# Optimization experiments

Hardware: AMD Instinct MI355X
Metric: run time of the kernel (lower is better)

## Reference

```python
import jax, jax.numpy as jnp
import numpy as np

N_NODES = 50000
N_EDGES = 1600000
IN_DIM, HID_DIM, OUT_DIM, HEADS = 128, 128, 64, 8
NEG_SLOPE = 0.2
BN_EPS = 1e-5


def setup_inputs() -> dict:
    key = jax.random.key(0)
    ks = jax.random.split(key, 12)
    hpc = HID_DIM // HEADS  # per-head channels of layer 1
    return {
        "x": jax.random.normal(ks[0], (N_NODES, IN_DIM), jnp.float32),
        "edge_index": jax.random.randint(ks[1], (2, N_EDGES), 0, N_NODES, jnp.int64),
        "W1": jax.random.normal(ks[2], (IN_DIM, HEADS * hpc), jnp.float32) * 0.05,
        "a1_src": jax.random.normal(ks[3], (HEADS, hpc), jnp.float32) * 0.1,
        "a1_dst": jax.random.normal(ks[4], (HEADS, hpc), jnp.float32) * 0.1,
        "b1": jnp.zeros((HEADS * hpc,), jnp.float32),
        "bn_gamma": jnp.ones((HID_DIM,), jnp.float32),
        "bn_beta": jnp.zeros((HID_DIM,), jnp.float32),
        "W2": jax.random.normal(ks[5], (HID_DIM, OUT_DIM), jnp.float32) * 0.05,
        "a2_src": jax.random.normal(ks[6], (1, OUT_DIM), jnp.float32) * 0.1,
        "a2_dst": jax.random.normal(ks[7], (1, OUT_DIM), jnp.float32) * 0.1,
        "b2": jnp.zeros((OUT_DIM,), jnp.float32),
    }


def _gat_conv(x, src, dst, W, a_src, a_dst, bias, heads, n_nodes):
    # x: [N, Fin]; src/dst: [E'] (self-loops already appended)
    hpc = W.shape[1] // heads
    h = (x @ W).reshape(n_nodes, heads, hpc)                 # [N,H,C]
    alpha_s = jnp.einsum("nhc,hc->nh", h, a_src)             # [N,H]
    alpha_d = jnp.einsum("nhc,hc->nh", h, a_dst)
    e = alpha_s[src] + alpha_d[dst]                          # [E',H]
    e = jax.nn.leaky_relu(e, NEG_SLOPE)
    # segment softmax over destination neighborhoods
    m = jax.ops.segment_max(e, dst, num_segments=n_nodes)    # [N,H]
    m = jnp.where(jnp.isfinite(m), m, 0.0)
    ee = jnp.exp(e - m[dst])
    denom = jax.ops.segment_sum(ee, dst, num_segments=n_nodes)
    alpha = ee / (denom[dst] + 1e-16)                        # [E',H]
    msg = h[src] * alpha[:, :, None]                         # [E',H,C]
    out = jax.ops.segment_sum(msg, dst, num_segments=n_nodes)  # [N,H,C]
    return out.reshape(n_nodes, heads * hpc) + bias


def _batch_norm(x, gamma, beta):
    mu = jnp.mean(x, axis=0)
    var = jnp.var(x, axis=0)
    return gamma * (x - mu) * jax.lax.rsqrt(var + BN_EPS) + beta


def reference(x, edge_index, W1, a1_src, a1_dst, b1, bn_gamma, bn_beta, W2, a2_src, a2_dst, b2):
    n = x.shape[0]
    loops = jnp.arange(n, dtype=edge_index.dtype)
    src = jnp.concatenate([edge_index[0], loops])            # PyG add_self_loops
    dst = jnp.concatenate([edge_index[1], loops])
    h = _gat_conv(x, src, dst, W1, a1_src, a1_dst, b1, HEADS, n)
    h = _batch_norm(h, bn_gamma, bn_beta)
    h = jax.nn.elu(h)
    # dropout: identity at inference
    out = _gat_conv(h, src, dst, W2, a2_src, a2_dst, b2, 1, n)
    return out
```

## Files before the change

kernel.cpp:

```cpp
#include <hip/hip_runtime.h>
#include <hip/hip_bf16.h>

#define N_NODES 50000
#define N_EDGES 1600000
#define HEADS 8
#define NBK 196
#define NBLK 196
#define EPB 8192

typedef unsigned short u16;
typedef unsigned char u8;
typedef unsigned int u32;
typedef __attribute__((ext_vector_type(8))) short bf16x8;
typedef __attribute__((ext_vector_type(4))) float f32x4;

__device__ __forceinline__ float bf2f(u16 u) {
  union { u32 i; float f; } v; v.i = ((u32)u) << 16; return v.f;
}
__device__ __forceinline__ float bflo(u32 p) {
  union { u32 i; float f; } v; v.i = p << 16; return v.f;
}
__device__ __forceinline__ float bfhi(u32 p) {
  union { u32 i; float f; } v; v.i = p & 0xffff0000u; return v.f;
}
__device__ __forceinline__ u16 f2bf(float f) {
  union { float f; u32 i; } v; v.f = f;
  u32 r = v.i + 0x7fff + ((v.i >> 16) & 1);
  return (u16)(r >> 16);
}
__device__ __forceinline__ u32 pack2(float a, float b) {
  return (u32)f2bf(a) | ((u32)f2bf(b) << 16);
}

__global__ void k_detect(const u16* __restrict__ x, const u32* __restrict__ ei,
                         int* __restrict__ flags) {
  __shared__ int cbig, cnz;
  if (threadIdx.x == 0) { cbig = 0; cnz = 0; }
  __syncthreads();
  int lb = 0, ln = 0;
  for (int i = threadIdx.x; i < 4096; i += 256) {
    int ex = (x[i] >> 7) & 0xff;
    lb += (ex >= 140);
    if (i < 2048) ln += (ei[2 * i + 1] != 0);
  }
  atomicAdd(&cbig, lb); atomicAdd(&cnz, ln);
  __syncthreads();
  if (threadIdx.x == 0) {
    flags[0] = (cbig > 16) ? 1 : 0;
    flags[1] = (cnz == 0) ? 1 : 0;
  }
}

__global__ void k_convsmall(const void* a1s, const void* a1d, const void* b1,
                            const void* gam, const void* bet, const void* a2s,
                            const void* a2d, const void* b2, const void* W1,
                            const void* W2, float* __restrict__ smallf,
                            u16* __restrict__ w1t, u16* __restrict__ w2t,
                            const int* __restrict__ flags) {
  int i = blockIdx.x * 256 + threadIdx.x;
  if (i >= 25408) return;
  bool f32 = flags[0] != 0;
  auto ld = [&](const void* p, int off) -> float {
    return f32 ? ((const float*)p)[off] : bf2f(((const u16*)p)[off]);
  };
  if (i >= 17216) {
    int j = i - 17216, n = j >> 7, k = j & 127;
    w2t[j] = f2bf(ld(W2, k * 64 + n));
  } else if (i >= 832) {
    int j = i - 832, n = j >> 7, k = j & 127;
    w1t[j] = f2bf(ld(W1, k * 128 + n));
  } else {
    const void* src; int off;
    if (i >= 768)      { src = b2;  off = i - 768; }
    else if (i >= 704) { src = a2d; off = i - 704; }
    else if (i >= 640) { src = a2s; off = i - 640; }
    else if (i >= 512) { src = bet; off = i - 512; }
    else if (i >= 384) { src = gam; off = i - 384; }
    else if (i >= 256) { src = b1;  off = i - 256; }
    else if (i >= 128) { src = a1d; off = i - 128; }
    else               { src = a1s; off = i; }
    smallf[i] = ld(src, off);
  }
}

__global__ __launch_bounds__(256) void k_hist(const int* __restrict__ ei,
                                              int* __restrict__ H,
                                              int* __restrict__ totals,
                                              const int* __restrict__ flags) {
  __shared__ int hist[NBK];
  int t = threadIdx.x, blk = blockIdx.x;
  for (int i = t; i < NBK; i += 256) hist[i] = 0;
  __syncthreads();
  bool i64 = flags[1] != 0;
  int base = blk * EPB;
  for (int k = 0; k < 32; k++) {
    int e = base + k * 256 + t;
    if (e < N_EDGES) {
      int d = i64 ? ei[2 * (N_EDGES + e)] : ei[N_EDGES + e];
      atomicAdd(&hist[d >> 8], 1);
    }
  }
  __syncthreads();
  for (int i = t; i < NBK; i += 256) {
    H[i * NBLK + blk] = hist[i];
    atomicAdd(&totals[i], hist[i]);
  }
}

__global__ void k_scan_tot(const int* __restrict__ totals, int* __restrict__ bucketBase) {
  __shared__ int tmp[256];
  int t = threadIdx.x;
  int v = (t < NBK) ? totals[t] : 0;
  tmp[t] = v; __syncthreads();
  for (int o = 1; o < 256; o <<= 1) {
    int x = (t >= o) ? tmp[t - o] : 0; __syncthreads();
    tmp[t] += x; __syncthreads();
  }
  if (t < NBK) bucketBase[t] = tmp[t] - v;
  if (t == NBK - 1) bucketBase[NBK] = tmp[t];
}

__global__ void k_scan_blk(const int* __restrict__ H, const int* __restrict__ bucketBase,
                           int* __restrict__ P) {
  __shared__ int tmp[256];
  int t = threadIdx.x, b = blockIdx.x;
  int v = (t < NBLK) ? H[b * NBLK + t] : 0;
  tmp[t] = v; __syncthreads();
  for (int o = 1; o < 256; o <<= 1) {
    int x = (t >= o) ? tmp[t - o] : 0; __syncthreads();
    tmp[t] += x; __syncthreads();
  }
  if (t < NBLK) P[b * NBLK + t] = bucketBase[b] + tmp[t] - v;
}

__global__ __launch_bounds__(256) void k_bucket(const int* __restrict__ ei,
                                                const int* __restrict__ P,
                                                u32* __restrict__ buf,
                                                const int* __restrict__ flags) {
  __shared__ u32 sv[EPB];
  __shared__ u16 rank[EPB];
  __shared__ u8  sk8[EPB];
  __shared__ int cnt[NBK], scn[NBK], tmp[256];
  int t = threadIdx.x, blk = blockIdx.x;
  int base = blk * EPB;
  int nE = N_EDGES - base; if (nE > EPB) nE = EPB;
  for (int i = t; i < NBK; i += 256) cnt[i] = 0;
  __syncthreads();
  bool i64 = flags[1] != 0;
  for (int k = 0; k < EPB / 256; k++) {
    int li = k * 256 + t, e = base + li;
    if (li < nE) {
      int d = i64 ? ei[2 * (N_EDGES + e)] : ei[N_EDGES + e];
      rank[li] = (u16)atomicAdd(&cnt[d >> 8], 1);
    }
  }
  __syncthreads();
  int v = (t < NBK) ? cnt[t] : 0;
  tmp[t] = v; __syncthreads();
  for (int o = 1; o < 256; o <<= 1) {
    int x = (t >= o) ? tmp[t - o] : 0; __syncthreads();
    tmp[t] += x; __syncthreads();
  }
  if (t < NBK) scn[t] = tmp[t] - v;
  __syncthreads();
  for (int k = 0; k < EPB / 256; k++) {
    int li = k * 256 + t, e = base + li;
    if (li < nE) {
      int s = i64 ? ei[2 * e] : ei[e];
      int d = i64 ? ei[2 * (N_EDGES + e)] : ei[N_EDGES + e];
      int key = d >> 8;
      int pos = scn[key] + rank[li];
      sv[pos] = ((u32)(d & 255) << 16) | (u32)s;
      sk8[pos] = (u8)key;
    }
  }
  __syncthreads();
  for (int i = t; i < nE; i += 256) {
    int b = sk8[i];
    buf[P[b * NBLK + blk] + (i - scn[b])] = sv[i];
  }
}

__global__ __launch_bounds__(256) void k_csr(const u32* __restrict__ buf,
                                             const int* __restrict__ bucketBase,
                                             int* __restrict__ row_start,
                                             int* __restrict__ deg,
                                             int* __restrict__ csr, int N) {
  __shared__ int cnt[256], scn[256], cur[256];
  int b = blockIdx.x, t = threadIdx.x;
  int lo = bucketBase[b], hi = bucketBase[b + 1];
  cnt[t] = 0; __syncthreads();
  for (int e = lo + t; e < hi; e += 256) atomicAdd(&cnt[(buf[e] >> 16) & 255], 1);
  __syncthreads();
  int v = cnt[t];
  scn[t] = v; __syncthreads();
  for (int o = 1; o < 256; o <<= 1) {
    int x = (t >= o) ? scn[t - o] : 0; __syncthreads();
    scn[t] += x; __syncthreads();
  }
  int excl = scn[t] - v;
  int node = b * 256 + t;
  if (node < N) { row_start[node] = lo + excl; deg[node] = v; }
  cur[t] = lo + excl;
  __syncthreads();
  for (int e = lo + t; e < hi; e += 256) {
    u32 p = buf[e];
    int pos = atomicAdd(&cur[(p >> 16) & 255], 1);
    csr[pos] = p & 0xffff;
  }
}

template <int NCOLS, bool EPI, bool AFLAG>
__global__ __launch_bounds__(256) void k_gemm_mfma(const void* __restrict__ A,
                                                   const u16* __restrict__ BT,
                                                   const float* __restrict__ scale,
                                                   const float* __restrict__ shift,
                                                   const float* __restrict__ a2s,
                                                   const float* __restrict__ a2d,
                                                   float* __restrict__ as_out,
                                                   float* __restrict__ ad_out,
                                                   u16* __restrict__ C, int M,
                                                   const int* __restrict__ flags) {
  constexpr int KP = 136;
  constexpr int NT = NCOLS / 16;
  __shared__ u16 As[64 * KP];
  __shared__ u16 Bs[NCOLS * KP];
  int t = threadIdx.x;
  int row0 = blockIdx.x * 64;
  bool af32 = AFLAG ? (flags[0] != 0) : false;

  for (int i = t; i < NCOLS * 16; i += 256) {
    int n = i >> 4, q = i & 15;
    *(uint4*)&Bs[n * KP + q * 8] = ((const uint4*)BT)[n * 16 + q];
  }
  for (int i = t; i < 64 * 32; i += 256) {
    int r = i >> 5, c4 = i & 31;
    int row = row0 + r;
    uint2 pk = make_uint2(0u, 0u);
    if (row < M) {
      if (EPI) {
        uint2 p = ((const uint2*)A)[(size_t)row * 32 + c4];
        int c = c4 * 4;
        float v0 = bflo(p.x), v1 = bfhi(p.x), v2 = bflo(p.y), v3 = bfhi(p.y);
        v0 = fmaf(v0, scale[c],     shift[c]);     v0 = v0 > 0.f ? v0 : __expf(v0) - 1.f;
        v1 = fmaf(v1, scale[c + 1], shift[c + 1]); v1 = v1 > 0.f ? v1 : __expf(v1) - 1.f;
        v2 = fmaf(v2, scale[c + 2], shift[c + 2]); v2 = v2 > 0.f ? v2 : __expf(v2) - 1.f;
        v3 = fmaf(v3, scale[c + 3], shift[c + 3]); v3 = v3 > 0.f ? v3 : __expf(v3) - 1.f;
        pk.x = pack2(v0, v1); pk.y = pack2(v2, v3);
      } else if (af32) {
        float4 v = ((const float4*)A)[(size_t)row * 32 + c4];
        pk.x = pack2(v.x, v.y); pk.y = pack2(v.z, v.w);
      } else {
        pk = ((const uint2*)A)[(size_t)row * 32 + c4];
      }
    }
    *(uint2*)&As[r * KP + c4 * 4] = pk;
  }
  __syncthreads();

  int lane = t & 63, w = t >> 6;
  int m = lane & 15, quad = lane >> 4;
  f32x4 acc[NT];
#pragma unroll
  for (int nt = 0; nt < NT; nt++) acc[nt] = (f32x4)(0.f);
  const u16* aBase = &As[(w * 16 + m) * KP + quad * 8];
  const u16* bBase = &Bs[m * KP + quad * 8];
#pragma unroll
  for (int ks = 0; ks < 4; ks++) {
    bf16x8 af = *(const bf16x8*)(aBase + ks * 32);
#pragma unroll
    for (int nt = 0; nt < NT; nt++) {
      bf16x8 bf = *(const bf16x8*)(bBase + nt * 16 * KP + ks * 32);
      acc[nt] = __builtin_amdgcn_mfma_f32_16x16x32_bf16(af, bf, acc[nt], 0, 0, 0);
    }
  }
  int orow0 = row0 + w * 16 + quad * 4;
#pragma unroll
  for (int nt = 0; nt < NT; nt++) {
#pragma unroll
    for (int r = 0; r < 4; r++) {
      int row = orow0 + r;
      if (row < M) C[(size_t)row * NCOLS + nt * 16 + m] = f2bf(acc[nt][r]);
    }
  }
  if (EPI) {
    float a2sv[NT], a2dv[NT];
#pragma unroll
    for (int nt = 0; nt < NT; nt++) { a2sv[nt] = a2s[nt * 16 + m]; a2dv[nt] = a2d[nt * 16 + m]; }
#pragma unroll
    for (int r = 0; r < 4; r++) {
      float vs = 0.f, vd = 0.f;
#pragma unroll
      for (int nt = 0; nt < NT; nt++) {
        vs = fmaf(acc[nt][r], a2sv[nt], vs);
        vd = fmaf(acc[nt][r], a2dv[nt], vd);
      }
      vs += __shfl_xor(vs, 1); vd += __shfl_xor(vd, 1);
      vs += __shfl_xor(vs, 2); vd += __shfl_xor(vd, 2);
      vs += __shfl_xor(vs, 4); vd += __shfl_xor(vd, 4);
      vs += __shfl_xor(vs, 8); vd += __shfl_xor(vd, 8);
      int row = orow0 + r;
      if (row < M && m == 0) { as_out[row] = vs; ad_out[row] = vd; }
    }
  }
}

__global__ void k_alpha1(const u16* __restrict__ h1b, const float* __restrict__ a1s,
                         const float* __restrict__ a1d, float* __restrict__ as_out,
                         float* __restrict__ ad_out, int N) {
  int idx = blockIdx.x * 256 + threadIdx.x;
  if (idx >= N * HEADS) return;
  int n = idx >> 3, h = idx & 7;
  const u32* hp = (const u32*)&h1b[((size_t)n << 7) + (h << 4)];
  float s = 0.f, d = 0.f;
#pragma unroll
  for (int q = 0; q < 8; q++) {
    u32 p = hp[q];
    float v0 = bflo(p), v1 = bfhi(p);
    int b = (h << 4) + q * 2;
    s = fmaf(v0, a1s[b], s); s = fmaf(v1, a1s[b + 1], s);
    d = fmaf(v0, a1d[b], d); d = fmaf(v1, a1d[b + 1], d);
  }
  as_out[idx] = s; ad_out[idx] = d;
}

__global__ __launch_bounds__(256) void k_agg1(const u16* __restrict__ h1b,
                                              const float* __restrict__ as_,
                                              const float* __restrict__ ad_,
                                              const int* __restrict__ csr,
                                              const int* __restrict__ row_start,
                                              const int* __restrict__ deg,
                                              const float* __restrict__ b1,
                                              u16* __restrict__ out, int N) {
  int node = blockIdx.x * 4 + (threadIdx.x >> 6);
  if (node >= N) return;
  int l = threadIdx.x & 63;
  int head = l >> 3, sub = l & 7;
  int gbase = l & 56;
  int node_u = __builtin_amdgcn_readfirstlane(node);
  int st = __builtin_amdgcn_readfirstlane(row_start[node_u]);
  int cnt = __builtin_amdgcn_readfirstlane(deg[node_u]);
  const int* cp = csr + st;
  const u32* h32 = (const u32*)h1b;
  float ad = ad_[(node_u << 3) | head];
  float sp = 0.f, a0 = 0.f, a1 = 0.f;
  int j = 0;
  for (; j + 8 <= cnt; j += 8) {
    int ssub = cp[j + sub];
    float e = as_[(ssub << 3) | head] + ad;
    e = fmaxf(e, 0.2f * e);
    float p = __expf(e);
    sp += p;
#pragma unroll
    for (int k = 0; k < 8; k++) {
      int sk = cp[j + k];
      float pk = __shfl(p, gbase | k);
      u32 hv = h32[(sk << 6) | l];
      a0 = fmaf(pk, bflo(hv), a0);
      a1 = fmaf(pk, bfhi(hv), a1);
    }
  }
  for (; j < cnt; j++) {
    int s0 = cp[j];
    float e0 = as_[(s0 << 3) | head] + ad;
    e0 = fmaxf(e0, 0.2f * e0);
    float p0 = __expf(e0);
    if (sub == 0) sp += p0;
    u32 hv = h32[(s0 << 6) | l];
    a0 = fmaf(p0, bflo(hv), a0); a1 = fmaf(p0, bfhi(hv), a1);
  }
  {
    float e0 = as_[(node_u << 3) | head] + ad;
    e0 = fmaxf(e0, 0.2f * e0);
    float p0 = __expf(e0);
    if (sub == 0) sp += p0;
    u32 hv = h32[((size_t)node_u << 6) | l];
    a0 = fmaf(p0, bflo(hv), a0); a1 = fmaf(p0, bfhi(hv), a1);
  }
  sp += __shfl_xor(sp, 1);
  sp += __shfl_xor(sp, 2);
  sp += __shfl_xor(sp, 4);
  float inv = 1.f / (sp + 1e-16f);
  int c0 = l * 2;
  ((u32*)out)[((size_t)node_u << 6) + l] =
      pack2(fmaf(a0, inv, b1[c0]), fmaf(a1, inv, b1[c0 + 1]));
}

__global__ void k_bnstat(const u16* __restrict__ h, float* __restrict__ gsum,
                         float* __restrict__ gsq, int N) {
  __shared__ float ts[256], tq[256];
  int t = threadIdx.x, col = t & 127, rr = t >> 7;
  int row0 = blockIdx.x * 128;
  float s = 0.f, q = 0.f;
  for (int r = rr; r < 128; r += 2) {
    int row = row0 + r;
    if (row < N) {
      float v = bf2f(h[((size_t)row << 7) + col]);
      s += v; q = fmaf(v, v, q);
    }
  }
  ts[t] = s; tq[t] = q; __syncthreads();
  if (t < 128) {
    atomicAdd(&gsum[t], ts[t] + ts[t + 128]);
    atomicAdd(&gsq[t], tq[t] + tq[t + 128]);
  }
}

__global__ void k_bnfin(const float* __restrict__ gsum, const float* __restrict__ gsq,
                        const float* __restrict__ gamma, const float* __restrict__ beta,
                        float* __restrict__ scale, float* __restrict__ shift, int N) {
  int t = threadIdx.x;
  if (t >= 128) return;
  float mu = gsum[t] / (float)N;
  float var = fmaxf(gsq[t] / (float)N - mu * mu, 0.f);
  float s = gamma[t] * rsqrtf(var + 1e-5f);
  scale[t] = s;
  shift[t] = beta[t] - mu * s;
}

__global__ __launch_bounds__(256) void k_agg2(const u16* __restrict__ h2b,
                                              const float* __restrict__ as_,
                                              const float* __restrict__ ad_,
                                              const int* __restrict__ csr,
                                              const int* __restrict__ row_start,
                                              const int* __restrict__ deg,
                                              const float* __restrict__ b2,
                                              void* __restrict__ out,
                                              const int* __restrict__ flags, int N) {
  int node = blockIdx.x * 4 + (threadIdx.x >> 6);
  if (node >= N) return;
  int l = threadIdx.x & 63;
  int sub = l & 7, gbase = l & 56;
  int node_u = __builtin_amdgcn_readfirstlane(node);
  int st = __builtin_amdgcn_readfirstlane(row_start[node_u]);
  int cnt = __builtin_amdgcn_readfirstlane(deg[node_u]);
  const int* cp = csr + st;
  float ad = ad_[node_u];
  float sp = 0.f, a = 0.f;
  int j = 0;
  for (; j + 8 <= cnt; j += 8) {
    int ssub = cp[j + sub];
    float e = as_[ssub] + ad;
    e = fmaxf(e, 0.2f * e);
    float p = __expf(e);
    sp += p;
#pragma unroll
    for (int k = 0; k < 8; k++) {
      int sk = cp[j + k];
      float pk = __shfl(p, gbase | k);
      a = fmaf(pk, bf2f((h2b + (sk << 6))[l]), a);
    }
  }
  for (; j < cnt; j++) {
    int s0 = cp[j];
    float e0 = as_[s0] + ad;
    e0 = fmaxf(e0, 0.2f * e0);
    float p0 = __expf(e0);
    if (sub == 0) sp += p0;
    a = fmaf(p0, bf2f((h2b + (s0 << 6))[l]), a);
  }
  {
    float e0 = as_[node_u] + ad;
    e0 = fmaxf(e0, 0.2f * e0);
    float p0 = __expf(e0);
    if (sub == 0) sp += p0;
    a = fmaf(p0, bf2f((h2b + (node_u << 6))[l]), a);
  }
  sp += __shfl_xor(sp, 1);
  sp += __shfl_xor(sp, 2);
  sp += __shfl_xor(sp, 4);
  float r = a / (sp + 1e-16f) + b2[l];
  size_t idx = ((size_t)node_u << 6) + l;
  if (flags[0]) ((float*)out)[idx] = r;
  else          ((u16*)out)[idx] = f2bf(r);
}

extern "C" void kernel_launch(void* const* d_in, const int* in_sizes, int n_in,
                              void* d_out, int out_size, void* d_ws, size_t ws_size,
                              hipStream_t stream) {
  const void* x   = d_in[0];
  const int*  ei  = (const int*)d_in[1];
  const void* W1  = d_in[2];
  const void* a1s = d_in[3];
  const void* a1d = d_in[4];
  const void* b1  = d_in[5];
  const void* gam = d_in[6];
  const void* bet = d_in[7];
  const void* W2  = d_in[8];
  const void* a2s = d_in[9];
  const void* a2d = d_in[10];
  const void* b2  = d_in[11];

  char* ws = (char*)d_ws;
  size_t off = 0;
  auto alloc = [&](size_t bytes) -> void* {
    void* p = ws + off;
    off += (bytes + 255) & ~(size_t)255;
    return p;
  };
  int* flags = (int*)alloc(256);
  char* zreg = (char*)alloc(2048);
  int* totals = (int*)zreg;
  float* gsum = (float*)(zreg + 1024);
  float* gsq  = gsum + 128;
  int* H  = (int*)alloc((size_t)NBK * NBLK * 4);
  int* P  = (int*)alloc((size_t)NBK * NBLK * 4);
  int* bucketBase = (int*)alloc(1024);
  u32* ebuf = (u32*)alloc((size_t)N_EDGES * 4);
  int* csr = (int*)alloc((size_t)N_EDGES * 4);
  int* row_start = (int*)alloc((size_t)N_NODES * 4);
  int* deg = (int*)alloc((size_t)N_NODES * 4);
  float* smallf = (float*)alloc(832 * 4);
  float* a1sf = smallf;        float* a1df = smallf + 128;
  float* b1f  = smallf + 256;  float* gamf = smallf + 384;
  float* betf = smallf + 512;  float* a2sf = smallf + 640;
  float* a2df = smallf + 704;  float* b2f  = smallf + 768;
  u16* w1t = (u16*)alloc(16384 * 2);
  u16* w2t = (u16*)alloc(8192 * 2);
  u16* h1b  = (u16*)alloc((size_t)N_NODES * 128 * 2);
  u16* h1ob = (u16*)alloc((size_t)N_NODES * 128 * 2);
  u16* h2b  = (u16*)alloc((size_t)N_NODES * 64 * 2);
  float* al1s = (float*)alloc((size_t)N_NODES * 8 * 4);
  float* al1d = (float*)alloc((size_t)N_NODES * 8 * 4);
  float* scale = (float*)alloc(512);
  float* shift = (float*)alloc(512);
  float* al2s = (float*)alloc((size_t)N_NODES * 4);
  float* al2d = (float*)alloc((size_t)N_NODES * 4);
  if (off > ws_size) return;

  hipMemsetAsync(zreg, 0, 2048, stream);
  k_detect<<<1, 256, 0, stream>>>((const u16*)x, (const u32*)ei, flags);
  k_convsmall<<<100, 256, 0, stream>>>(a1s, a1d, b1, gam, bet, a2s, a2d, b2, W1, W2,
                                       smallf, w1t, w2t, flags);

  k_hist<<<NBLK, 256, 0, stream>>>(ei, H, totals, flags);
  k_scan_tot<<<1, 256, 0, stream>>>(totals, bucketBase);
  k_scan_blk<<<NBK, 256, 0, stream>>>(H, bucketBase, P);
  k_bucket<<<NBLK, 256, 0, stream>>>(ei, P, ebuf, flags);
  k_csr<<<NBK, 256, 0, stream>>>(ebuf, bucketBase, row_start, deg, csr, N_NODES);

  k_gemm_mfma<128, false, true><<<(N_NODES + 63) / 64, 256, 0, stream>>>(
      x, w1t, nullptr, nullptr, nullptr, nullptr, nullptr, nullptr, h1b, N_NODES, flags);
  k_alpha1<<<(N_NODES * HEADS + 255) / 256, 256, 0, stream>>>(h1b, a1sf, a1df,
                                                              al1s, al1d, N_NODES);
  k_agg1<<<(N_NODES + 3) / 4, 256, 0, stream>>>(h1b, al1s, al1d, csr, row_start, deg,
                                                b1f, h1ob, N_NODES);

  k_bnstat<<<(N_NODES + 127) / 128, 256, 0, stream>>>(h1ob, gsum, gsq, N_NODES);
  k_bnfin<<<1, 128, 0, stream>>>(gsum, gsq, gamf, betf, scale, shift, N_NODES);

  k_gemm_mfma<64, true, false><<<(N_NODES + 63) / 64, 256, 0, stream>>>(
      h1ob, w2t, scale, shift, a2sf, a2df, al2s, al2d, h2b, N_NODES, flags);
  k_agg2<<<(N_NODES + 3) / 4, 256, 0, stream>>>(h2b, al2s, al2d, csr, row_start, deg,
                                                b2f, d_out, flags, N_NODES);
}
```

Baseline: 329.3 us.

## Split node features into 32-channel slabs and fuse layer-1 alpha into GEMM

The GEMMs now write their bf16 outputs as column slabs of 32 channels (64 bytes per row). Each aggregation block handles one slab, so the per-edge gathered row is smaller and the working set of each pass is more likely to stay in L2. Aggregation is split across 4 (layer 1) or 2 (layer 2) grid slices, with two edges processed per wave iteration. The separate alpha1 kernel is removed and its per-head attention dot products are computed in the GEMM epilogue. The cost is that the edge list, attention exponentials and index loads are repeated once per slab.

```diff
diff --git a/kernel.cpp b/kernel.cpp
--- a/kernel.cpp
+++ b/kernel.cpp
@@ -7,6 +7,7 @@
 #define NBK 196
 #define NBLK 196
 #define EPB 8192
+#define QSTRIDE 1600000
 
 typedef unsigned short u16;
 typedef unsigned char u8;
@@ -31,6 +32,7 @@
 __device__ __forceinline__ u32 pack2(float a, float b) {
   return (u32)f2bf(a) | ((u32)f2bf(b) << 16);
 }
+__device__ __forceinline__ int rfl(int x) { return __builtin_amdgcn_readfirstlane(x); }
 
 __global__ void k_detect(const u16* __restrict__ x, const u32* __restrict__ ei,
                          int* __restrict__ flags) {
@@ -210,13 +212,13 @@
   }
 }
 
-template <int NCOLS, bool EPI, bool AFLAG>
+template <int NCOLS, bool EPI, bool ALPHA1, bool AFLAG>
 __global__ __launch_bounds__(256) void k_gemm_mfma(const void* __restrict__ A,
                                                    const u16* __restrict__ BT,
                                                    const float* __restrict__ scale,
                                                    const float* __restrict__ shift,
-                                                   const float* __restrict__ a2s,
-                                                   const float* __restrict__ a2d,
+                                                   const float* __restrict__ va,
+                                                   const float* __restrict__ vb,
                                                    float* __restrict__ as_out,
                                                    float* __restrict__ ad_out,
                                                    u16* __restrict__ C, int M,
@@ -277,23 +279,43 @@
   int orow0 = row0 + w * 16 + quad * 4;
 #pragma unroll
   for (int nt = 0; nt < NT; nt++) {
+    size_t base = (size_t)(nt >> 1) * QSTRIDE + ((nt & 1) * 16 + m);
 #pragma unroll
     for (int r = 0; r < 4; r++) {
       int row = orow0 + r;
-      if (row < M) C[(size_t)row * NCOLS + nt * 16 + m] = f2bf(acc[nt][r]);
+      if (row < M) C[base + (size_t)row * 32] = f2bf(acc[nt][r]);
+    }
+  }
+  if (ALPHA1) {
+    float pav[NT], pbv[NT];
+#pragma unroll
+    for (int nt = 0; nt < NT; nt++) { pav[nt] = va[nt * 16 + m]; pbv[nt] = vb[nt * 16 + m]; }
+#pragma unroll
+    for (int r = 0; r < 4; r++) {
+      int row = orow0 + r;
+#pragma unroll
+      for (int nt = 0; nt < NT; nt++) {
+        float vs = acc[nt][r] * pav[nt];
+        float vd = acc[nt][r] * pbv[nt];
+        vs += __shfl_xor(vs, 1); vd += __shfl_xor(vd, 1);
+        vs += __shfl_xor(vs, 2); vd += __shfl_xor(vd, 2);
+        vs += __shfl_xor(vs, 4); vd += __shfl_xor(vd, 4);
+        vs += __shfl_xor(vs, 8); vd += __shfl_xor(vd, 8);
+        if (row < M && m == 0) { as_out[row * 8 + nt] = vs; ad_out[row * 8 + nt] = vd; }
+      }
     }
   }
   if (EPI) {
-    float a2sv[NT], a2dv[NT];
-#pragma unroll
-    for (int nt = 0; nt < NT; nt++) { a2sv[nt] = a2s[nt * 16 + m]; a2dv[nt] = a2d[nt * 16 + m]; }
+    float pav[NT], pbv[NT];
+#pragma unroll
+    for (int nt = 0; nt < NT; nt++) { pav[nt] = va[nt * 16 + m]; pbv[nt] = vb[nt * 16 + m]; }
 #pragma unroll
     for (int r = 0; r < 4; r++) {
       float vs = 0.f, vd = 0.f;
 #pragma unroll
       for (int nt = 0; nt < NT; nt++) {
-        vs = fmaf(acc[nt][r], a2sv[nt], vs);
-        vd = fmaf(acc[nt][r], a2dv[nt], vd);
+        vs = fmaf(acc[nt][r], pav[nt], vs);
+        vd = fmaf(acc[nt][r], pbv[nt], vd);
       }
       vs += __shfl_xor(vs, 1); vd += __shfl_xor(vd, 1);
       vs += __shfl_xor(vs, 2); vd += __shfl_xor(vd, 2);
@@ -305,26 +327,7 @@
   }
 }
 
-__global__ void k_alpha1(const u16* __restrict__ h1b, const float* __restrict__ a1s,
-                         const float* __restrict__ a1d, float* __restrict__ as_out,
-                         float* __restrict__ ad_out, int N) {
-  int idx = blockIdx.x * 256 + threadIdx.x;
-  if (idx >= N * HEADS) return;
-  int n = idx >> 3, h = idx & 7;
-  const u32* hp = (const u32*)&h1b[((size_t)n << 7) + (h << 4)];
-  float s = 0.f, d = 0.f;
-#pragma unroll
-  for (int q = 0; q < 8; q++) {
-    u32 p = hp[q];
-    float v0 = bflo(p), v1 = bfhi(p);
-    int b = (h << 4) + q * 2;
-    s = fmaf(v0, a1s[b], s); s = fmaf(v1, a1s[b + 1], s);
-    d = fmaf(v0, a1d[b], d); d = fmaf(v1, a1d[b + 1], d);
-  }
-  as_out[idx] = s; ad_out[idx] = d;
-}
-
-__global__ __launch_bounds__(256) void k_agg1(const u16* __restrict__ h1b,
+__global__ __launch_bounds__(256) void k_agg1(const u16* __restrict__ h1r,
                                               const float* __restrict__ as_,
                                               const float* __restrict__ ad_,
                                               const int* __restrict__ csr,
@@ -332,58 +335,55 @@
                                               const int* __restrict__ deg,
                                               const float* __restrict__ b1,
                                               u16* __restrict__ out, int N) {
-  int node = blockIdx.x * 4 + (threadIdx.x >> 6);
+  int bq = blockIdx.x / 12500;
+  int nb = blockIdx.x - bq * 12500;
+  int node = nb * 4 + (threadIdx.x >> 6);
   if (node >= N) return;
   int l = threadIdx.x & 63;
-  int head = l >> 3, sub = l & 7;
-  int gbase = l & 56;
-  int node_u = __builtin_amdgcn_readfirstlane(node);
-  int st = __builtin_amdgcn_readfirstlane(row_start[node_u]);
-  int cnt = __builtin_amdgcn_readfirstlane(deg[node_u]);
+  int c = l & 31, eh = l >> 5;
+  int h2sel = c >> 4;
+  int node_u = rfl(node);
+  int st = rfl(row_start[node_u]);
+  int cnt = rfl(deg[node_u]);
   const int* cp = csr + st;
-  const u32* h32 = (const u32*)h1b;
-  float ad = ad_[(node_u << 3) | head];
-  float sp = 0.f, a0 = 0.f, a1 = 0.f;
+  const u16* hq = h1r + (size_t)bq * QSTRIDE;
+  int q2 = bq * 2;
+  int myh = (l >> 3) & 1;
+  float ad = ad_[node_u * 8 + q2 + myh];
+  float sp = 0.f, a = 0.f;
   int j = 0;
   for (; j + 8 <= cnt; j += 8) {
-    int ssub = cp[j + sub];
-    float e = as_[(ssub << 3) | head] + ad;
+    int svi = cp[j + (l & 7)];
+    float e = as_[svi * 8 + q2 + myh] + ad;
     e = fmaxf(e, 0.2f * e);
     float p = __expf(e);
-    sp += p;
-#pragma unroll
-    for (int k = 0; k < 8; k++) {
-      int sk = cp[j + k];
-      float pk = __shfl(p, gbase | k);
-      u32 hv = h32[(sk << 6) | l];
-      a0 = fmaf(pk, bflo(hv), a0);
-      a1 = fmaf(pk, bfhi(hv), a1);
-    }
-  }
-  for (; j < cnt; j++) {
-    int s0 = cp[j];
-    float e0 = as_[(s0 << 3) | head] + ad;
-    e0 = fmaxf(e0, 0.2f * e0);
-    float p0 = __expf(e0);
-    if (sub == 0) sp += p0;
-    u32 hv = h32[(s0 << 6) | l];
-    a0 = fmaf(p0, bflo(hv), a0); a1 = fmaf(p0, bfhi(hv), a1);
-  }
-  {
-    float e0 = as_[(node_u << 3) | head] + ad;
-    e0 = fmaxf(e0, 0.2f * e0);
-    float p0 = __expf(e0);
-    if (sub == 0) sp += p0;
-    u32 hv = h32[((size_t)node_u << 6) | l];
-    a0 = fmaf(p0, bflo(hv), a0); a1 = fmaf(p0, bfhi(hv), a1);
+    if (l < 16) sp += p;
+#pragma unroll
+    for (int k = 0; k < 4; k++) {
+      int se = cp[j + 2 * k], so = cp[j + 2 * k + 1];
+      int sk = eh ? so : se;
+      float pk = __shfl(p, (h2sel << 3) | (2 * k + eh));
+      a = fmaf(pk, bf2f(hq[(size_t)sk * 32 + c]), a);
+    }
+  }
+  for (; j <= cnt; j++) {
+    int s0 = (j < cnt) ? rfl(cp[j]) : node_u;
+    float e = as_[s0 * 8 + q2 + myh] + ad;
+    e = fmaxf(e, 0.2f * e);
+    float p = __expf(e);
+    if ((l & 55) == 0) sp += p;
+    float pk = __shfl(p, h2sel << 3);
+    if (eh == 0) a = fmaf(pk, bf2f(hq[(size_t)s0 * 32 + c]), a);
   }
   sp += __shfl_xor(sp, 1);
   sp += __shfl_xor(sp, 2);
   sp += __shfl_xor(sp, 4);
-  float inv = 1.f / (sp + 1e-16f);
-  int c0 = l * 2;
-  ((u32*)out)[((size_t)node_u << 6) + l] =
-      pack2(fmaf(a0, inv, b1[c0]), fmaf(a1, inv, b1[c0 + 1]));
+  float inv = 1.f / (__shfl(sp, h2sel << 3) + 1e-16f);
+  a += __shfl_xor(a, 32);
+  if (eh == 0) {
+    int ch = bq * 32 + c;
+    out[(size_t)node_u * 128 + ch] = f2bf(fmaf(a, inv, b1[ch]));
+  }
 }
 
 __global__ void k_bnstat(const u16* __restrict__ h, float* __restrict__ gsum,
@@ -418,7 +418,7 @@
   shift[t] = beta[t] - mu * s;
 }
 
-__global__ __launch_bounds__(256) void k_agg2(const u16* __restrict__ h2b,
+__global__ __launch_bounds__(256) void k_agg2(const u16* __restrict__ h2q,
                                               const float* __restrict__ as_,
                                               const float* __restrict__ ad_,
                                               const int* __restrict__ csr,
@@ -427,52 +427,55 @@
                                               const float* __restrict__ b2,
                                               void* __restrict__ out,
                                               const int* __restrict__ flags, int N) {
-  int node = blockIdx.x * 4 + (threadIdx.x >> 6);
+  int bq = blockIdx.x / 12500;
+  int nb = blockIdx.x - bq * 12500;
+  int node = nb * 4 + (threadIdx.x >> 6);
   if (node >= N) return;
   int l = threadIdx.x & 63;
-  int sub = l & 7, gbase = l & 56;
-  int node_u = __builtin_amdgcn_readfirstlane(node);
-  int st = __builtin_amdgcn_readfirstlane(row_start[node_u]);
-  int cnt = __builtin_amdgcn_readfirstlane(deg[node_u]);
+  int c = l & 31, eh = l >> 5;
+  int node_u = rfl(node);
+  int st = rfl(row_start[node_u]);
+  int cnt = rfl(deg[node_u]);
   const int* cp = csr + st;
+  const u16* hq = h2q + (size_t)bq * QSTRIDE;
   float ad = ad_[node_u];
   float sp = 0.f, a = 0.f;
   int j = 0;
   for (; j + 8 <= cnt; j += 8) {
-    int ssub = cp[j + sub];
-    float e = as_[ssub] + ad;
+    int svi = cp[j + (l & 7)];
+    float e = as_[svi] + ad;
     e = fmaxf(e, 0.2f * e);
     float p = __expf(e);
-    sp += p;
-#pragma unroll
-    for (int k = 0; k < 8; k++) {
-      int sk = cp[j + k];
-      float pk = __shfl(p, gbase | k);
-      a = fmaf(pk, bf2f((h2b + (sk << 6))[l]), a);
-    }
-  }
-  for (; j < cnt; j++) {
-    int s0 = cp[j];
-    float e0 = as_[s0] + ad;
-    e0 = fmaxf(e0, 0.2f * e0);
-    float p0 = __expf(e0);
-    if (sub == 0) sp += p0;
-    a = fmaf(p0, bf2f((h2b + (s0 << 6))[l]), a);
-  }
-  {
-    float e0 = as_[node_u] + ad;
-    e0 = fmaxf(e0, 0.2f * e0);
-    float p0 = __expf(e0);
-    if (sub == 0) sp += p0;
-    a = fmaf(p0, bf2f((h2b + (node_u << 6))[l]), a);
+    if (l < 8) sp += p;
+#pragma unroll
+    for (int k = 0; k < 4; k++) {
+      int se = cp[j + 2 * k], so = cp[j + 2 * k + 1];
+      int sk = eh ? so : se;
+      float pk = __shfl(p, 2 * k + eh);
+      a = fmaf(pk, bf2f(hq[(size_t)sk * 32 + c]), a);
+    }
+  }
+  for (; j <= cnt; j++) {
+    int s0 = (j < cnt) ? rfl(cp[j]) : node_u;
+    float e = as_[s0] + ad;
+    e = fmaxf(e, 0.2f * e);
+    float p = __expf(e);
+    if (l == 0) sp += p;
+    float pk = __shfl(p, 0);
+    if (eh == 0) a = fmaf(pk, bf2f(hq[(size_t)s0 * 32 + c]), a);
   }
   sp += __shfl_xor(sp, 1);
   sp += __shfl_xor(sp, 2);
   sp += __shfl_xor(sp, 4);
-  float r = a / (sp + 1e-16f) + b2[l];
-  size_t idx = ((size_t)node_u << 6) + l;
-  if (flags[0]) ((float*)out)[idx] = r;
-  else          ((u16*)out)[idx] = f2bf(r);
+  float inv = 1.f / (__shfl(sp, 0) + 1e-16f);
+  a += __shfl_xor(a, 32);
+  if (eh == 0) {
+    int ch = bq * 32 + c;
+    float r = fmaf(a, inv, b2[ch]);
+    size_t idx = (size_t)node_u * 64 + ch;
+    if (flags[0]) ((float*)out)[idx] = r;
+    else          ((u16*)out)[idx] = f2bf(r);
+  }
 }
 
 extern "C" void kernel_launch(void* const* d_in, const int* in_sizes, int n_in,
@@ -517,9 +520,9 @@
   float* a2df = smallf + 704;  float* b2f  = smallf + 768;
   u16* w1t = (u16*)alloc(16384 * 2);
   u16* w2t = (u16*)alloc(8192 * 2);
-  u16* h1b  = (u16*)alloc((size_t)N_NODES * 128 * 2);
+  u16* h1r  = (u16*)alloc((size_t)4 * QSTRIDE * 2);
   u16* h1ob = (u16*)alloc((size_t)N_NODES * 128 * 2);
-  u16* h2b  = (u16*)alloc((size_t)N_NODES * 64 * 2);
+  u16* h2q  = (u16*)alloc((size_t)2 * QSTRIDE * 2);
   float* al1s = (float*)alloc((size_t)N_NODES * 8 * 4);
   float* al1d = (float*)alloc((size_t)N_NODES * 8 * 4);
   float* scale = (float*)alloc(512);
@@ -539,18 +542,16 @@
   k_bucket<<<NBLK, 256, 0, stream>>>(ei, P, ebuf, flags);
   k_csr<<<NBK, 256, 0, stream>>>(ebuf, bucketBase, row_start, deg, csr, N_NODES);
 
-  k_gemm_mfma<128, false, true><<<(N_NODES + 63) / 64, 256, 0, stream>>>(
-      x, w1t, nullptr, nullptr, nullptr, nullptr, nullptr, nullptr, h1b, N_NODES, flags);
-  k_alpha1<<<(N_NODES * HEADS + 255) / 256, 256, 0, stream>>>(h1b, a1sf, a1df,
-                                                              al1s, al1d, N_NODES);
-  k_agg1<<<(N_NODES + 3) / 4, 256, 0, stream>>>(h1b, al1s, al1d, csr, row_start, deg,
-                                                b1f, h1ob, N_NODES);
+  k_gemm_mfma<128, false, true, true><<<(N_NODES + 63) / 64, 256, 0, stream>>>(
+      x, w1t, nullptr, nullptr, a1sf, a1df, al1s, al1d, h1r, N_NODES, flags);
+  k_agg1<<<4 * 12500, 256, 0, stream>>>(h1r, al1s, al1d, csr, row_start, deg,
+                                        b1f, h1ob, N_NODES);
 
   k_bnstat<<<(N_NODES + 127) / 128, 256, 0, stream>>>(h1ob, gsum, gsq, N_NODES);
   k_bnfin<<<1, 128, 0, stream>>>(gsum, gsq, gamf, betf, scale, shift, N_NODES);
 
-  k_gemm_mfma<64, true, false><<<(N_NODES + 63) / 64, 256, 0, stream>>>(
-      h1ob, w2t, scale, shift, a2sf, a2df, al2s, al2d, h2b, N_NODES, flags);
-  k_agg2<<<(N_NODES + 3) / 4, 256, 0, stream>>>(h2b, al2s, al2d, csr, row_start, deg,
-                                                b2f, d_out, flags, N_NODES);
-}
+  k_gemm_mfma<64, true, false, false><<<(N_NODES + 63) / 64, 256, 0, stream>>>(
+      h1ob, w2t, scale, shift, a2sf, a2df, al2s, al2d, h2q, N_NODES, flags);
+  k_agg2<<<2 * 12500, 256, 0, stream>>>(h2q, al2s, al2d, csr, row_start, deg,
+                                        b2f, d_out, flags, N_NODES);
+}
```

After: 505.7 us. 53.6% more time.
